# Kernel optimization log

Measured on AMD Instinct MI355X. Metric: run time of the kernel, lower is better.

## Reference

```python
import jax, jax.numpy as jnp
import numpy as np

B, D_IN, D_H = 32768, 512, 512


def setup_inputs() -> dict:
    key = jax.random.key(0)
    ks = jax.random.split(key, 7)
    s_in = 1.0 / np.sqrt(D_IN)
    s_h = 1.0 / np.sqrt(D_H)
    x = jax.random.normal(ks[0], (B, D_IN), dtype=jnp.float32)
    C = jax.random.normal(ks[1], (B, D_H), dtype=jnp.float32)
    h = jax.random.normal(ks[2], (B, D_H), dtype=jnp.float32)
    # Concatenated gate weights: order [i, f, o, g]. Each gate has its own
    # independent Linear(input_dim->hidden) and Linear(hidden->hidden) in torch;
    # stacking them column-wise gives identical math with 2 GEMMs.
    Wx = jax.random.uniform(ks[3], (D_IN, 4 * D_H), dtype=jnp.float32, minval=-s_in, maxval=s_in)
    bx = jax.random.uniform(ks[4], (4 * D_H,), dtype=jnp.float32, minval=-s_in, maxval=s_in)
    Wh = jax.random.uniform(ks[5], (D_H, 4 * D_H), dtype=jnp.float32, minval=-s_h, maxval=s_h)
    bh = jax.random.uniform(ks[6], (4 * D_H,), dtype=jnp.float32, minval=-s_h, maxval=s_h)
    return {"x": x, "C": C, "h": h, "Wx": Wx, "bx": bx, "Wh": Wh, "bh": bh}


def reference(x, C, h, Wx, bx, Wh, bh):
    # Two fused GEMMs replace the 8 small Linear calls (same math).
    z = x @ Wx + bx + h @ Wh + bh  # [B, 4H]
    i, f, o, g = jnp.split(z, 4, axis=-1)
    i = jax.nn.sigmoid(i)
    f = jax.nn.sigmoid(f)
    o = jax.nn.sigmoid(o)
    g = jnp.tanh(g)
    C_new = f * C + i * g
    h_new = o * jnp.tanh(C_new)
    return (C_new, h_new)
```

## Files before the change

### kernel.cpp

```cpp
#include <hip/hip_runtime.h>
#include <stdint.h>


#define BROWS 32768
#define DH 512
#define KTOT 1024
#define BM 128
#define BK 64

typedef __attribute__((ext_vector_type(8))) __bf16 bf16x8;
typedef __attribute__((ext_vector_type(4))) float f32x4;
typedef __attribute__((address_space(1))) void gvoid;
typedef __attribute__((address_space(3))) void lvoid;

__device__ __forceinline__ void gl_lds16(const void* g, void* l) {
  __builtin_amdgcn_global_load_lds((gvoid*)g, (lvoid*)l, 16, 0, 0);
}

__device__ __forceinline__ float sigf(float v)  { return 1.0f / (1.0f + __expf(-v)); }
__device__ __forceinline__ float tanhf_(float v){ return 1.0f - 2.0f / (1.0f + __expf(2.0f * v)); }

__global__ void conv_xh(const float* __restrict__ x, const float* __restrict__ h,
                        __bf16* __restrict__ xh) {
  int o = blockIdx.x * 256 + threadIdx.x;
  int c = (o & 127) * 8;
  int r = o >> 7;
  const float* src = (c < DH) ? (x + (size_t)r * DH + c)
                              : (h + (size_t)r * DH + (c - DH));
  float4 f0 = *(const float4*)src;
  float4 f1 = *(const float4*)(src + 4);
  bf16x8 v;
  v[0] = (__bf16)f0.x; v[1] = (__bf16)f0.y; v[2] = (__bf16)f0.z; v[3] = (__bf16)f0.w;
  v[4] = (__bf16)f1.x; v[5] = (__bf16)f1.y; v[6] = (__bf16)f1.z; v[7] = (__bf16)f1.w;
  *(bf16x8*)(xh + (size_t)o * 8) = v;
}

__global__ void pack_w(const float* __restrict__ Wx, const float* __restrict__ Wh,
                       __bf16* __restrict__ Wt) {
  __shared__ __bf16 T[128][72];
  const int jb = blockIdx.y;
  const int k0 = blockIdx.x * 64;
  const float* Wsrc = (k0 < DH) ? (Wx + (size_t)k0 * 4 * DH)
                                : (Wh + (size_t)(k0 - DH) * 4 * DH);
  const int t = threadIdx.x;
  const int s = t & 31, kr0 = t >> 5;
  const int g = s >> 3, q = s & 7;
  const int r0 = (q >> 2) * 64 + g * 16 + (q & 3) * 4;
  #pragma unroll
  for (int it = 0; it < 8; ++it) {
    int kr = it * 8 + kr0;
    float4 f = *(const float4*)(Wsrc + (size_t)kr * 4 * DH + g * DH + jb * 32 + q * 4);
    T[r0 + 0][kr] = (__bf16)f.x;
    T[r0 + 1][kr] = (__bf16)f.y;
    T[r0 + 2][kr] = (__bf16)f.z;
    T[r0 + 3][kr] = (__bf16)f.w;
  }
  __syncthreads();
  #pragma unroll
  for (int it = 0; it < 4; ++it) {
    int lin = it * 256 + t;
    int r = lin >> 3, k8 = lin & 7;
    bf16x8 v;
    #pragma unroll
    for (int j = 0; j < 8; ++j) v[j] = T[r][k8 * 8 + j];
    *(bf16x8*)(Wt + (size_t)(jb * 128 + r) * KTOT + k0 + k8 * 8) = v;
  }
}

__global__ __launch_bounds__(256, 3) void lstm_gemm2(
    const __bf16* __restrict__ xh, const __bf16* __restrict__ Wt,
    const float* __restrict__ bx, const float* __restrict__ bh,
    const float* __restrict__ Cin, float* __restrict__ out) {
  __shared__ __attribute__((aligned(16))) __bf16 As[BM * BK];
  __shared__ __attribute__((aligned(16))) __bf16 Bs[BM * BK];

  const int tid  = threadIdx.x;
  const int lane = tid & 63;
  const int wave = tid >> 6;
  const int wm = wave >> 1, wn = wave & 1;
  const int jb   = blockIdx.x;
  const int row0 = blockIdx.y * BM;

  const __bf16* Bt = Wt + (size_t)jb * 128 * KTOT;

  const int hd = jb * 32 + wn * 16 + (lane & 15);
  float bias[4], cpv[4][4];
  #pragma unroll
  for (int g = 0; g < 4; ++g) bias[g] = bx[g * DH + hd] + bh[g * DH + hd];
  #pragma unroll
  for (int cm = 0; cm < 4; ++cm)
    #pragma unroll
    for (int i2 = 0; i2 < 4; ++i2)
      cpv[cm][i2] = Cin[(size_t)(row0 + wm * 64 + cm * 16 + (lane >> 4) * 4 + i2) * DH + hd];

  f32x4 acc[4][4];
  #pragma unroll
  for (int a_ = 0; a_ < 4; ++a_)
    #pragma unroll
    for (int b_ = 0; b_ < 4; ++b_) acc[a_][b_] = (f32x4)0.0f;

  for (int k0 = 0; k0 < KTOT; k0 += BK) {
    #pragma unroll
    for (int it = 0; it < 4; ++it) {
      int lin = it * 256 + tid;
      int r = lin >> 3, c8 = lin & 7;
      int cs = c8 ^ (r & 7);
      gl_lds16(xh + (size_t)(row0 + r) * KTOT + k0 + cs * 8, &As[lin * 8]);
    }
    #pragma unroll
    for (int it = 0; it < 4; ++it) {
      int lin = it * 256 + tid;
      int r = lin >> 3, c8 = lin & 7;
      int cs = c8 ^ (r & 7);
      gl_lds16(Bt + (size_t)r * KTOT + k0 + cs * 8, &Bs[lin * 8]);
    }
    __syncthreads();

    #pragma unroll
    for (int ks = 0; ks < 2; ++ks) {
      const int q = lane >> 4;
      bf16x8 af[4], bfr[4];
      #pragma unroll
      for (int cm = 0; cm < 4; ++cm) {
        int row = wm * 64 + cm * 16 + (lane & 15);
        int cc = (ks * 4 + q) ^ (row & 7);
        af[cm] = *(const bf16x8*)&As[row * BK + cc * 8];
      }
      #pragma unroll
      for (int cn = 0; cn < 4; ++cn) {
        int row = wn * 64 + cn * 16 + (lane & 15);
        int cc = (ks * 4 + q) ^ (row & 7);
        bfr[cn] = *(const bf16x8*)&Bs[row * BK + cc * 8];
      }
      #pragma unroll
      for (int cm = 0; cm < 4; ++cm)
        #pragma unroll
        for (int cn = 0; cn < 4; ++cn)
          acc[cm][cn] = __builtin_amdgcn_mfma_f32_16x16x32_bf16(
              af[cm], bfr[cn], acc[cm][cn], 0, 0, 0);
    }
    __syncthreads();
  }

  #pragma unroll
  for (int cm = 0; cm < 4; ++cm) {
    const int rbase = row0 + wm * 64 + cm * 16 + (lane >> 4) * 4;
    #pragma unroll
    for (int i2 = 0; i2 < 4; ++i2) {
      const size_t r = (size_t)(rbase + i2);
      float ig = sigf(acc[cm][0][i2] + bias[0]);
      float fg = sigf(acc[cm][1][i2] + bias[1]);
      float og = sigf(acc[cm][2][i2] + bias[2]);
      float gg = tanhf_(acc[cm][3][i2] + bias[3]);
      float cnew = fg * cpv[cm][i2] + ig * gg;
      float hnew = og * tanhf_(cnew);
      out[r * DH + hd] = cnew;
      out[(size_t)BROWS * DH + r * DH + hd] = hnew;
    }
  }
}

__global__ __launch_bounds__(256, 3) void lstm_gemm(
    const float* __restrict__ x, const float* __restrict__ h,
    const __bf16* __restrict__ Wt, const float* __restrict__ bx,
    const float* __restrict__ bh, const float* __restrict__ Cin,
    float* __restrict__ out) {
  __shared__ __attribute__((aligned(16))) __bf16 As[BM * BK];
  __shared__ __attribute__((aligned(16))) __bf16 Bs[BM * BK];
  const int tid  = threadIdx.x;
  const int lane = tid & 63;
  const int wave = tid >> 6;
  const int wm = wave >> 1, wn = wave & 1;
  const int jb   = blockIdx.x;
  const int row0 = blockIdx.y * BM;
  const __bf16* Bt = Wt + (size_t)jb * 128 * KTOT;
  f32x4 acc[4][4];
  #pragma unroll
  for (int a_ = 0; a_ < 4; ++a_)
    #pragma unroll
    for (int b_ = 0; b_ < 4; ++b_) acc[a_][b_] = (f32x4)0.0f;
  for (int k0 = 0; k0 < KTOT; k0 += BK) {
    const float* Aptr = (k0 < DH) ? (x + (size_t)row0 * DH + k0)
                                  : (h + (size_t)row0 * DH + (k0 - DH));
    bf16x8 ta[4], tb[4];
    #pragma unroll
    for (int it = 0; it < 4; ++it) {
      int lin = it * 256 + tid;
      int r = lin >> 3, c8 = lin & 7;
      const float* src = Aptr + r * DH + c8 * 8;
      float4 f0 = *(const float4*)src;
      float4 f1 = *(const float4*)(src + 4);
      bf16x8 v;
      v[0] = (__bf16)f0.x; v[1] = (__bf16)f0.y; v[2] = (__bf16)f0.z; v[3] = (__bf16)f0.w;
      v[4] = (__bf16)f1.x; v[5] = (__bf16)f1.y; v[6] = (__bf16)f1.z; v[7] = (__bf16)f1.w;
      ta[it] = v;
      tb[it] = *(const bf16x8*)(Bt + (size_t)r * KTOT + k0 + c8 * 8);
    }
    #pragma unroll
    for (int it = 0; it < 4; ++it) {
      int lin = it * 256 + tid;
      *(bf16x8*)&As[lin * 8] = ta[it];
      *(bf16x8*)&Bs[lin * 8] = tb[it];
    }
    __syncthreads();
    #pragma unroll
    for (int ks = 0; ks < 2; ++ks) {
      const int ko = ks * 32 + (lane >> 4) * 8;
      bf16x8 af[4], bfr[4];
      #pragma unroll
      for (int cm = 0; cm < 4; ++cm)
        af[cm] = *(const bf16x8*)&As[(wm * 64 + cm * 16 + (lane & 15)) * BK + ko];
      #pragma unroll
      for (int cn = 0; cn < 4; ++cn)
        bfr[cn] = *(const bf16x8*)&Bs[(wn * 64 + cn * 16 + (lane & 15)) * BK + ko];
      #pragma unroll
      for (int cm = 0; cm < 4; ++cm)
        #pragma unroll
        for (int cn = 0; cn < 4; ++cn)
          acc[cm][cn] = __builtin_amdgcn_mfma_f32_16x16x32_bf16(
              af[cm], bfr[cn], acc[cm][cn], 0, 0, 0);
    }
    __syncthreads();
  }
  const int hd = jb * 32 + wn * 16 + (lane & 15);
  float bias[4];
  #pragma unroll
  for (int g2 = 0; g2 < 4; ++g2) bias[g2] = bx[g2 * DH + hd] + bh[g2 * DH + hd];
  #pragma unroll
  for (int cm = 0; cm < 4; ++cm) {
    const int rbase = row0 + wm * 64 + cm * 16 + (lane >> 4) * 4;
    #pragma unroll
    for (int i2 = 0; i2 < 4; ++i2) {
      const size_t r = (size_t)(rbase + i2);
      float ig = sigf(acc[cm][0][i2] + bias[0]);
      float fg = sigf(acc[cm][1][i2] + bias[1]);
      float og = sigf(acc[cm][2][i2] + bias[2]);
      float gg = tanhf_(acc[cm][3][i2] + bias[3]);
      float cp = Cin[r * DH + hd];
      float cnew = fg * cp + ig * gg;
      float hnew = og * tanhf_(cnew);
      out[r * DH + hd] = cnew;
      out[(size_t)BROWS * DH + r * DH + hd] = hnew;
    }
  }
}

__global__ void lstm_naive(const float* __restrict__ x, const float* __restrict__ Cin,
                           const float* __restrict__ h, const float* __restrict__ Wx,
                           const float* __restrict__ bxp, const float* __restrict__ Wh,
                           const float* __restrict__ bhp, float* __restrict__ out) {
  int idx = blockIdx.x * 256 + threadIdx.x;
  int r = idx >> 9, hd = idx & 511;
  float z[4];
  #pragma unroll
  for (int g = 0; g < 4; ++g) z[g] = bxp[g * DH + hd] + bhp[g * DH + hd];
  for (int k = 0; k < DH; ++k) {
    float xv = x[(size_t)r * DH + k];
    #pragma unroll
    for (int g = 0; g < 4; ++g) z[g] += xv * Wx[k * 4 * DH + g * DH + hd];
  }
  for (int k = 0; k < DH; ++k) {
    float hv = h[(size_t)r * DH + k];
    #pragma unroll
    for (int g = 0; g < 4; ++g) z[g] += hv * Wh[k * 4 * DH + g * DH + hd];
  }
  float ig = sigf(z[0]), fg = sigf(z[1]), og = sigf(z[2]), gg = tanhf_(z[3]);
  float cp = Cin[(size_t)r * DH + hd];
  float cnew = fg * cp + ig * gg;
  float hnew = og * tanhf_(cnew);
  out[(size_t)r * DH + hd] = cnew;
  out[(size_t)BROWS * DH + (size_t)r * DH + hd] = hnew;
}

extern "C" void kernel_launch(void* const* d_in, const int* in_sizes, int n_in,
                              void* d_out, int out_size, void* d_ws, size_t ws_size,
                              hipStream_t stream) {
  const float* x  = (const float*)d_in[0];
  const float* Ci = (const float*)d_in[1];
  const float* h  = (const float*)d_in[2];
  const float* Wx = (const float*)d_in[3];
  const float* bx = (const float*)d_in[4];
  const float* Wh = (const float*)d_in[5];
  const float* bh = (const float*)d_in[6];
  float* out = (float*)d_out;

  const size_t wt_bytes = (size_t)2048 * KTOT * sizeof(__bf16);
  const size_t xh_bytes = (size_t)BROWS * KTOT * sizeof(__bf16);

  if (ws_size >= wt_bytes + xh_bytes) {
    __bf16* Wt = (__bf16*)d_ws;
    __bf16* xh = (__bf16*)((char*)d_ws + wt_bytes);
    pack_w<<<dim3(16, 16), dim3(256), 0, stream>>>(Wx, Wh, Wt);
    conv_xh<<<dim3((BROWS * KTOT / 8) / 256), dim3(256), 0, stream>>>(x, h, xh);
    lstm_gemm2<<<dim3(16, BROWS / BM), dim3(256), 0, stream>>>(xh, Wt, bx, bh, Ci, out);
  } else if (ws_size >= wt_bytes) {
    __bf16* Wt = (__bf16*)d_ws;
    pack_w<<<dim3(16, 16), dim3(256), 0, stream>>>(Wx, Wh, Wt);
    lstm_gemm<<<dim3(16, BROWS / BM), dim3(256), 0, stream>>>(x, h, Wt, bx, bh, Ci, out);
  } else {
    lstm_naive<<<dim3((BROWS * DH) / 256), dim3(256), 0, stream>>>(
        x, Ci, h, Wx, bx, Wh, bh, out);
  }
}
```

Baseline: 422.8 us.

## Merge weight pack and input conversion into one prep kernel, remap GEMM tiles

```diff
diff --git a/kernel.cpp b/kernel.cpp
--- a/kernel.cpp
+++ b/kernel.cpp
@@ -20,29 +20,12 @@
 __device__ __forceinline__ float sigf(float v)  { return 1.0f / (1.0f + __expf(-v)); }
 __device__ __forceinline__ float tanhf_(float v){ return 1.0f - 2.0f / (1.0f + __expf(2.0f * v)); }
 
-__global__ void conv_xh(const float* __restrict__ x, const float* __restrict__ h,
-                        __bf16* __restrict__ xh) {
-  int o = blockIdx.x * 256 + threadIdx.x;
-  int c = (o & 127) * 8;
-  int r = o >> 7;
-  const float* src = (c < DH) ? (x + (size_t)r * DH + c)
-                              : (h + (size_t)r * DH + (c - DH));
-  float4 f0 = *(const float4*)src;
-  float4 f1 = *(const float4*)(src + 4);
-  bf16x8 v;
-  v[0] = (__bf16)f0.x; v[1] = (__bf16)f0.y; v[2] = (__bf16)f0.z; v[3] = (__bf16)f0.w;
-  v[4] = (__bf16)f1.x; v[5] = (__bf16)f1.y; v[6] = (__bf16)f1.z; v[7] = (__bf16)f1.w;
-  *(bf16x8*)(xh + (size_t)o * 8) = v;
-}
-
-__global__ void pack_w(const float* __restrict__ Wx, const float* __restrict__ Wh,
-                       __bf16* __restrict__ Wt) {
-  __shared__ __bf16 T[128][72];
-  const int jb = blockIdx.y;
-  const int k0 = blockIdx.x * 64;
+__device__ __forceinline__ void pack_w_body(const float* __restrict__ Wx,
+                                            const float* __restrict__ Wh,
+                                            __bf16* __restrict__ Wt,
+                                            __bf16 (*T)[72], int jb, int k0, int t) {
   const float* Wsrc = (k0 < DH) ? (Wx + (size_t)k0 * 4 * DH)
                                 : (Wh + (size_t)(k0 - DH) * 4 * DH);
-  const int t = threadIdx.x;
   const int s = t & 31, kr0 = t >> 5;
   const int g = s >> 3, q = s & 7;
   const int r0 = (q >> 2) * 64 + g * 16 + (q & 3) * 4;
@@ -67,6 +50,49 @@
   }
 }
 
+#define PREP_PACK_BLOCKS 256
+#define PREP_CONV_BLOCKS 2048
+__global__ __launch_bounds__(256) void prep(
+    const float* __restrict__ x, const float* __restrict__ h,
+    const float* __restrict__ Wx, const float* __restrict__ Wh,
+    __bf16* __restrict__ xh, __bf16* __restrict__ Wt) {
+  __shared__ __bf16 T[128][72];
+  const int t = threadIdx.x;
+  if (blockIdx.x < PREP_PACK_BLOCKS) {
+    const int jb = blockIdx.x >> 4;
+    const int k0 = (blockIdx.x & 15) * 64;
+    pack_w_body(Wx, Wh, Wt, T, jb, k0, t);
+    return;
+  }
+  const int bid = blockIdx.x - PREP_PACK_BLOCKS;
+  const int64_t total  = (int64_t)BROWS * (KTOT / 16);
+  const int64_t stride = (int64_t)PREP_CONV_BLOCKS * 256;
+  for (int64_t i = (int64_t)bid * 256 + t; i < total; i += stride) {
+    const int64_t r = i >> 6;
+    const int c = (int)(i & 63) * 16;
+    const float* src = (c < DH) ? (x + r * DH + c)
+                                : (h + r * DH + (c - DH));
+    float4 f0 = *(const float4*)(src + 0);
+    float4 f1 = *(const float4*)(src + 4);
+    float4 f2 = *(const float4*)(src + 8);
+    float4 f3 = *(const float4*)(src + 12);
+    bf16x8 v0, v1;
+    v0[0] = (__bf16)f0.x; v0[1] = (__bf16)f0.y; v0[2] = (__bf16)f0.z; v0[3] = (__bf16)f0.w;
+    v0[4] = (__bf16)f1.x; v0[5] = (__bf16)f1.y; v0[6] = (__bf16)f1.z; v0[7] = (__bf16)f1.w;
+    v1[0] = (__bf16)f2.x; v1[1] = (__bf16)f2.y; v1[2] = (__bf16)f2.z; v1[3] = (__bf16)f2.w;
+    v1[4] = (__bf16)f3.x; v1[5] = (__bf16)f3.y; v1[6] = (__bf16)f3.z; v1[7] = (__bf16)f3.w;
+    bf16x8* dst = (bf16x8*)(xh + r * KTOT + c);
+    __builtin_nontemporal_store(v0, dst);
+    __builtin_nontemporal_store(v1, dst + 1);
+  }
+}
+
+__global__ void pack_w(const float* __restrict__ Wx, const float* __restrict__ Wh,
+                       __bf16* __restrict__ Wt) {
+  __shared__ __bf16 T[128][72];
+  pack_w_body(Wx, Wh, Wt, T, blockIdx.y, blockIdx.x * 64, threadIdx.x);
+}
+
 __global__ __launch_bounds__(256, 3) void lstm_gemm2(
     const __bf16* __restrict__ xh, const __bf16* __restrict__ Wt,
     const float* __restrict__ bx, const float* __restrict__ bh,
@@ -78,8 +104,11 @@
   const int lane = tid & 63;
   const int wave = tid >> 6;
   const int wm = wave >> 1, wn = wave & 1;
-  const int jb   = blockIdx.x;
-  const int row0 = blockIdx.y * BM;
+
+  const int wgid = blockIdx.y * 16 + blockIdx.x;
+  const int lin  = (wgid & 7) * 512 + (wgid >> 3);
+  const int jb   = lin & 15;
+  const int row0 = (lin >> 4) * BM;
 
   const __bf16* Bt = Wt + (size_t)jb * 128 * KTOT;
 
@@ -102,17 +131,17 @@
   for (int k0 = 0; k0 < KTOT; k0 += BK) {
     #pragma unroll
     for (int it = 0; it < 4; ++it) {
-      int lin = it * 256 + tid;
-      int r = lin >> 3, c8 = lin & 7;
+      int lin2 = it * 256 + tid;
+      int r = lin2 >> 3, c8 = lin2 & 7;
       int cs = c8 ^ (r & 7);
-      gl_lds16(xh + (size_t)(row0 + r) * KTOT + k0 + cs * 8, &As[lin * 8]);
+      gl_lds16(xh + (size_t)(row0 + r) * KTOT + k0 + cs * 8, &As[lin2 * 8]);
     }
     #pragma unroll
     for (int it = 0; it < 4; ++it) {
-      int lin = it * 256 + tid;
-      int r = lin >> 3, c8 = lin & 7;
+      int lin2 = it * 256 + tid;
+      int r = lin2 >> 3, c8 = lin2 & 7;
       int cs = c8 ^ (r & 7);
-      gl_lds16(Bt + (size_t)r * KTOT + k0 + cs * 8, &Bs[lin * 8]);
+      gl_lds16(Bt + (size_t)r * KTOT + k0 + cs * 8, &Bs[lin2 * 8]);
     }
     __syncthreads();
 
@@ -154,8 +183,8 @@
       float gg = tanhf_(acc[cm][3][i2] + bias[3]);
       float cnew = fg * cpv[cm][i2] + ig * gg;
       float hnew = og * tanhf_(cnew);
-      out[r * DH + hd] = cnew;
-      out[(size_t)BROWS * DH + r * DH + hd] = hnew;
+      __builtin_nontemporal_store(cnew, &out[r * DH + hd]);
+      __builtin_nontemporal_store(hnew, &out[(size_t)BROWS * DH + r * DH + hd]);
     }
   }
 }
@@ -165,8 +194,8 @@
     const __bf16* __restrict__ Wt, const float* __restrict__ bx,
     const float* __restrict__ bh, const float* __restrict__ Cin,
     float* __restrict__ out) {
-  __shared__ __attribute__((aligned(16))) __bf16 As[BM * BK];
-  __shared__ __attribute__((aligned(16))) __bf16 Bs[BM * BK];
+  __shared__ __attribute__((aligned(16))) __bf16 Asf[BM * BK];
+  __shared__ __attribute__((aligned(16))) __bf16 Bsf[BM * BK];
   const int tid  = threadIdx.x;
   const int lane = tid & 63;
   const int wave = tid >> 6;
@@ -199,8 +228,8 @@
     #pragma unroll
     for (int it = 0; it < 4; ++it) {
       int lin = it * 256 + tid;
-      *(bf16x8*)&As[lin * 8] = ta[it];
-      *(bf16x8*)&Bs[lin * 8] = tb[it];
+      *(bf16x8*)&Asf[lin * 8] = ta[it];
+      *(bf16x8*)&Bsf[lin * 8] = tb[it];
     }
     __syncthreads();
     #pragma unroll
@@ -209,10 +238,10 @@
       bf16x8 af[4], bfr[4];
       #pragma unroll
       for (int cm = 0; cm < 4; ++cm)
-        af[cm] = *(const bf16x8*)&As[(wm * 64 + cm * 16 + (lane & 15)) * BK + ko];
+        af[cm] = *(const bf16x8*)&Asf[(wm * 64 + cm * 16 + (lane & 15)) * BK + ko];
       #pragma unroll
       for (int cn = 0; cn < 4; ++cn)
-        bfr[cn] = *(const bf16x8*)&Bs[(wn * 64 + cn * 16 + (lane & 15)) * BK + ko];
+        bfr[cn] = *(const bf16x8*)&Bsf[(wn * 64 + cn * 16 + (lane & 15)) * BK + ko];
       #pragma unroll
       for (int cm = 0; cm < 4; ++cm)
         #pragma unroll
@@ -290,8 +319,8 @@
   if (ws_size >= wt_bytes + xh_bytes) {
     __bf16* Wt = (__bf16*)d_ws;
     __bf16* xh = (__bf16*)((char*)d_ws + wt_bytes);
-    pack_w<<<dim3(16, 16), dim3(256), 0, stream>>>(Wx, Wh, Wt);
-    conv_xh<<<dim3((BROWS * KTOT / 8) / 256), dim3(256), 0, stream>>>(x, h, xh);
+    prep<<<dim3(PREP_PACK_BLOCKS + PREP_CONV_BLOCKS), dim3(256), 0, stream>>>(
+        x, h, Wx, Wh, xh, Wt);
     lstm_gemm2<<<dim3(16, BROWS / BM), dim3(256), 0, stream>>>(xh, Wt, bx, bh, Ci, out);
   } else if (ws_size >= wt_bytes) {
     __bf16* Wt = (__bf16*)d_ws;
```

Measured after the change: 446.0 us. +5.5%, slower.
